# Kernel optimization log

Measured on AMD Instinct MI355X. Metric: run time of the kernel, lower is better.

Reference implementation:

```python
import jax, jax.numpy as jnp
import numpy as np

N = 100000   # nodes
E = 1600000  # edges
R = 8        # relations
B = 8        # bases (min(R, hidden))
IN = 128; HID = 128; OUT = 128
BN_EPS = 1e-5


def setup_inputs() -> dict:
    key = jax.random.key(0)
    ks = jax.random.split(key, 20)
    s = 0.1  # xavier-ish small gain as in reset_parameters
    f32 = jnp.float32
    inp = {
        'x': jax.random.normal(ks[0], (N, IN), f32),
        'edge_index': jax.random.randint(ks[1], (2, E), 0, N, dtype=jnp.int32),
        'edge_type': jax.random.randint(ks[2], (E,), 0, R, dtype=jnp.int32),
        # RGCNConv layer 1 (basis decomposition)
        'basis1': jax.random.normal(ks[3], (B, IN, HID), f32) * s,
        'comp1': jax.random.normal(ks[4], (R, B), f32) * s,
        'root1': jax.random.normal(ks[5], (IN, HID), f32) * s,
        'bias1': jnp.zeros((HID,), f32),
        # layer 2
        'basis2': jax.random.normal(ks[6], (B, HID, HID), f32) * s,
        'comp2': jax.random.normal(ks[7], (R, B), f32) * s,
        'root2': jax.random.normal(ks[8], (HID, HID), f32) * s,
        'bias2': jnp.zeros((HID,), f32),
        # layer 3
        'basis3': jax.random.normal(ks[9], (B, HID, OUT), f32) * s,
        'comp3': jax.random.normal(ks[10], (R, B), f32) * s,
        'root3': jax.random.normal(ks[11], (HID, OUT), f32) * s,
        'bias3': jnp.zeros((OUT,), f32),
        # BatchNorm affine params (batch-stat normalization)
        'bn1_gamma': jnp.ones((HID,), f32),
        'bn1_beta': jnp.zeros((HID,), f32),
        'bn2_gamma': jnp.ones((HID,), f32),
        'bn2_beta': jnp.zeros((HID,), f32),
    }
    return inp


def rgcn_conv(x, basis, comp, root, bias, src, dst, etype):
    # relation weights from basis decomposition: W[r] = sum_b comp[r,b] * basis[b]
    W = jnp.einsum('rb,bio->rio', comp, basis)  # [R, in, out]
    # mean aggregation per (dst, relation); transform after mean (linearity)
    seg = dst.astype(jnp.int32) * R + etype.astype(jnp.int32)  # [E]
    msg_sum = jax.ops.segment_sum(x[src], seg, num_segments=N * R)  # [N*R, in]
    cnt = jax.ops.segment_sum(jnp.ones((src.shape[0],), x.dtype), seg, num_segments=N * R)
    mean = msg_sum / jnp.maximum(cnt, 1.0)[:, None]
    mean = mean.reshape(N, R, -1)  # [N, R, in]
    out = jnp.einsum('nri,rio->no', mean, W) + x @ root + bias
    return out


def batchnorm(h, gamma, beta):
    m = h.mean(axis=0)
    v = h.var(axis=0)
    return (h - m) * jax.lax.rsqrt(v + BN_EPS) * gamma + beta


def reference(x, edge_index, edge_type,
              basis1, comp1, root1, bias1,
              basis2, comp2, root2, bias2,
              basis3, comp3, root3, bias3,
              bn1_gamma, bn1_beta, bn2_gamma, bn2_beta):
    src, dst = edge_index[0], edge_index[1]
    h = rgcn_conv(x, basis1, comp1, root1, bias1, src, dst, edge_type)
    h = batchnorm(h, bn1_gamma, bn1_beta)
    h = jnp.where(h > 0, h, 0.1 * h)  # LeakyReLU(0.1); dropout inactive (eval)
    h = rgcn_conv(h, basis2, comp2, root2, bias2, src, dst, edge_type)
    h = batchnorm(h, bn2_gamma, bn2_beta)
    h = jnp.where(h > 0, h, 0.1 * h)
    h = rgcn_conv(h, basis3, comp3, root3, bias3, src, dst, edge_type)
    # F.normalize(p=2, dim=1)
    norm = jnp.maximum(jnp.sqrt(jnp.sum(h * h, axis=1, keepdims=True)), 1e-12)
    return h / norm
```

## Files before the change

kernel.cpp:

```cpp
#include <hip/hip_runtime.h>

#define NN 100000
#define EE 1600000
#define RRR 8
#define NSEG (NN*RRR)
#define F 128
#define KDIM 1152
#define NKT 36
#define BNEPS 1e-5f

typedef __attribute__((ext_vector_type(8))) short bf16x8;
typedef __attribute__((ext_vector_type(8))) unsigned short u16x8;
typedef __attribute__((ext_vector_type(4))) float f32x4;

static __device__ __forceinline__ unsigned short bf16r(float f) {
  unsigned u = __float_as_uint(f);
  u += 0x7fffu + ((u >> 16) & 1u);
  return (unsigned short)(u >> 16);
}
static __device__ __forceinline__ float b2f(unsigned short s) {
  return __uint_as_float((unsigned)s << 16);
}

__global__ __launch_bounds__(256) void k_precnt(const float* __restrict__ x,
    unsigned short* __restrict__ xb, const int* __restrict__ dst,
    const int* __restrict__ et, unsigned* __restrict__ cnt) {
  int idx = blockIdx.x*256 + threadIdx.x;
  if (idx < NN*32) {
    float4 v = ((const float4*)x)[idx];
    ushort4 o;
    o.x = bf16r(v.x); o.y = bf16r(v.y); o.z = bf16r(v.z); o.w = bf16r(v.w);
    ((ushort4*)xb)[idx] = o;
  }
  if (idx < EE)
    atomicAdd(&cnt[dst[idx]*RRR + et[idx]], 1u);
}

__global__ void k_scan1(const unsigned* __restrict__ cnt, unsigned* __restrict__ off,
                        unsigned* __restrict__ bsum) {
  __shared__ unsigned s[256];
  int t = threadIdx.x;
  int base = blockIdx.x*2048 + t*8;
  unsigned loc[8];
  unsigned tot = 0;
#pragma unroll
  for (int j = 0; j < 8; j++) {
    unsigned v = (base+j < NSEG) ? cnt[base+j] : 0u;
    loc[j] = tot;
    tot += v;
  }
  s[t] = tot;
  __syncthreads();
  for (int d = 1; d < 256; d <<= 1) {
    unsigned v = (t >= d) ? s[t-d] : 0u;
    __syncthreads();
    s[t] += v;
    __syncthreads();
  }
  unsigned tbase = s[t] - tot;
#pragma unroll
  for (int j = 0; j < 8; j++)
    if (base+j < NSEG) off[base+j] = tbase + loc[j];
  if (t == 255) bsum[blockIdx.x] = s[255];
}

__global__ void k_scan2(unsigned* bsum, int nb) {
  __shared__ unsigned s[512];
  int t = threadIdx.x;
  unsigned v = (t < nb) ? bsum[t] : 0u;
  s[t] = v;
  __syncthreads();
  for (int d = 1; d < 512; d <<= 1) {
    unsigned u = (t >= d) ? s[t-d] : 0u;
    __syncthreads();
    s[t] += u;
    __syncthreads();
  }
  if (t < nb) bsum[t] = (t == 0) ? 0u : s[t-1];
}

__global__ void k_scan3(unsigned* off, const unsigned* __restrict__ bsum) {
  int i = blockIdx.x*256 + threadIdx.x;
  if (i < NSEG) off[i] += bsum[i >> 11];
}

__global__ void k_fill(const int* __restrict__ src, const int* __restrict__ dst,
                       const int* __restrict__ et, unsigned* __restrict__ off,
                       int* __restrict__ csr) {
  int e = blockIdx.x*256 + threadIdx.x;
  if (e < EE) {
    int seg = dst[e]*RRR + et[e];
    unsigned pos = atomicAdd(&off[seg], 1u);
    csr[pos] = src[e];
  }
}

__global__ void k_makeW3(const float* __restrict__ b1, const float* __restrict__ c1,
                         const float* __restrict__ r1, const float* __restrict__ b2,
                         const float* __restrict__ c2, const float* __restrict__ r2,
                         const float* __restrict__ b3, const float* __restrict__ c3,
                         const float* __restrict__ r3, unsigned short* __restrict__ WB3,
                         float* __restrict__ stats) {
  int kt = blockIdx.x, ct = blockIdx.y, l = blockIdx.z;
  int lane = threadIdx.x;
  if (kt == 0 && ct == 0 && l == 0) {
#pragma unroll
    for (int j = 0; j < 8; j++) stats[lane*8 + j] = 0.f;
  }
  const float* basis = (l == 0) ? b1 : (l == 1) ? b2 : b3;
  const float* comp  = (l == 0) ? c1 : (l == 1) ? c2 : c3;
  const float* root  = (l == 0) ? r1 : (l == 1) ? r2 : r3;
  int o = ct*16 + (lane & 15);
  int kbase = kt*32 + (lane >> 4)*8;
  unsigned short v[8];
#pragma unroll
  for (int j = 0; j < 8; j++) {
    int k = kbase + j;
    float val;
    if (k < 1024) {
      int r = k >> 7, i = k & 127;
      val = 0.f;
#pragma unroll
      for (int bb = 0; bb < 8; bb++)
        val += comp[r*8+bb] * basis[(bb*F + i)*F + o];
    } else {
      val = root[(k - 1024)*F + o];
    }
    v[j] = bf16r(val);
  }
  unsigned short* dstp = WB3 + (size_t)l*KDIM*F + ((size_t)(kt*8 + ct)*64 + lane)*8;
#pragma unroll
  for (int j = 0; j < 8; j++) dstp[j] = v[j];
}

__global__ __launch_bounds__(256) void k_agg(const unsigned short* __restrict__ hb,
    const unsigned* __restrict__ off, const unsigned* __restrict__ cnt,
    const int* __restrict__ csr, unsigned short* __restrict__ Mean,
    const float* __restrict__ stats, const float* __restrict__ gamma,
    const float* __restrict__ beta, int nodeBase, int hasBN) {
  int t = threadIdx.x;
  int sl = t & 15, c8 = sl*8;
  int g = t >> 4;
  int nl = blockIdx.x*4 + (g & 3);
  int node = nodeBase + nl;
  int rp = g >> 2;
  float sc[8], sh[8];
  float lk = hasBN ? 0.1f : 1.0f;
  if (hasBN) {
    const float invN = 1.f/(float)NN;
#pragma unroll
    for (int u = 0; u < 8; u++) {
      float m = stats[c8+u]*invN;
      float var = stats[128+c8+u]*invN - m*m;
      float rs = rsqrtf(var + BNEPS);
      float gg = gamma[c8+u]*rs;
      sc[u] = gg;
      sh[u] = beta[c8+u] - m*gg;
    }
  } else {
#pragma unroll
    for (int u = 0; u < 8; u++) { sc[u] = 1.f; sh[u] = 0.f; }
  }
  int s0 = node*RRR + 2*rp;
  unsigned cA = cnt[s0], cB = cnt[s0+1];
  unsigned bA = off[s0] - cA, bB = off[s0+1] - cB;
  const unsigned short* hc = hb + c8;
  float aA[8], aB[8];
#pragma unroll
  for (int u = 0; u < 8; u++) { aA[u] = 0.f; aB[u] = 0.f; }
  unsigned jA = 0, jB = 0;
  while (jA < cA || jB < cB) {
    unsigned nA = cA - jA; if (nA > 2) nA = 2;
    unsigned nB = cB - jB; if (nB > 2) nB = 2;
    int i0 = 0, i1 = 0, i2 = 0, i3 = 0;
    if (nA > 0) i0 = csr[bA + jA];
    if (nA > 1) i1 = csr[bA + jA + 1];
    if (nB > 0) i2 = csr[bB + jB];
    if (nB > 1) i3 = csr[bB + jB + 1];
    if (nA > 0) {
      u16x8 v = *(const u16x8*)&hc[(size_t)i0*F];
#pragma unroll
      for (int u = 0; u < 8; u++) { float z = b2f(v[u])*sc[u]+sh[u]; aA[u] += fmaxf(z, lk*z); }
    }
    if (nA > 1) {
      u16x8 v = *(const u16x8*)&hc[(size_t)i1*F];
#pragma unroll
      for (int u = 0; u < 8; u++) { float z = b2f(v[u])*sc[u]+sh[u]; aA[u] += fmaxf(z, lk*z); }
    }
    if (nB > 0) {
      u16x8 v = *(const u16x8*)&hc[(size_t)i2*F];
#pragma unroll
      for (int u = 0; u < 8; u++) { float z = b2f(v[u])*sc[u]+sh[u]; aB[u] += fmaxf(z, lk*z); }
    }
    if (nB > 1) {
      u16x8 v = *(const u16x8*)&hc[(size_t)i3*F];
#pragma unroll
      for (int u = 0; u < 8; u++) { float z = b2f(v[u])*sc[u]+sh[u]; aB[u] += fmaxf(z, lk*z); }
    }
    jA += nA; jB += nB;
  }
  float ivA = cA ? 1.f/(float)cA : 0.f;
  float ivB = cB ? 1.f/(float)cB : 0.f;
  u16x8 oA, oB;
#pragma unroll
  for (int u = 0; u < 8; u++) { oA[u] = bf16r(aA[u]*ivA); oB[u] = bf16r(aB[u]*ivB); }
  int ktl = sl >> 2, kgl = sl & 3;
  int rt = nl >> 4;
  int lraw = (nl & 15) + 16*kgl;
  size_t ciA = ((size_t)(rt*NKT + (2*rp  )*4 + ktl)*64 + lraw)*8;
  size_t ciB = ((size_t)(rt*NKT + (2*rp+1)*4 + ktl)*64 + lraw)*8;
  *(u16x8*)&Mean[ciA] = oA;
  *(u16x8*)&Mean[ciB] = oB;
  if (rp == 0) {
    u16x8 v = *(const u16x8*)&hc[(size_t)node*F];
    u16x8 os;
#pragma unroll
    for (int u = 0; u < 8; u++) {
      float z = b2f(v[u])*sc[u] + sh[u];
      os[u] = bf16r(fmaxf(z, lk*z));
    }
    size_t cs = ((size_t)(rt*NKT + 32 + ktl)*64 + lraw)*8;
    *(u16x8*)&Mean[cs] = os;
  }
}

__global__ __launch_bounds__(256) void k_gemm(const unsigned short* __restrict__ Mean,
    const unsigned short* __restrict__ WB, const float* __restrict__ bias,
    unsigned short* __restrict__ houtb, float* __restrict__ foutp,
    float* __restrict__ stats, int outBase, int count, int mode) {
  __shared__ float s_sum[128];
  __shared__ float s_sq[128];
  int t = threadIdx.x;
  int wave = t >> 6;
  int lane = t & 63;
  int rt = blockIdx.x*4 + wave;
  int rbase = rt*16;
  int rlo = lane & 15;
  int kg = lane >> 4;
  const unsigned short* ap = Mean + ((size_t)rt*NKT*64 + lane)*8;
  const unsigned short* bp = WB + (size_t)lane*8;

  if (mode == 0 && t < 128) { s_sum[t] = 0.f; s_sq[t] = 0.f; }

  f32x4 acc[8];
#pragma unroll
  for (int j = 0; j < 8; j++) acc[j] = (f32x4){0.f,0.f,0.f,0.f};

  for (int kt = 0; kt < NKT; kt++) {
    bf16x8 a = *(const bf16x8*)(ap + (size_t)kt*512);
#pragma unroll
    for (int ct = 0; ct < 8; ct++) {
      bf16x8 b = *(const bf16x8*)(bp + (size_t)(kt*8 + ct)*512);
      acc[ct] = __builtin_amdgcn_mfma_f32_16x16x32_bf16(a, b, acc[ct], 0, 0, 0);
    }
  }

  float bv[8];
#pragma unroll
  for (int ct = 0; ct < 8; ct++) bv[ct] = bias[ct*16 + rlo];

  if (mode == 0) {
    __syncthreads();
    float psum[8], psq[8];
#pragma unroll
    for (int ct = 0; ct < 8; ct++) { psum[ct] = 0.f; psq[ct] = 0.f; }
#pragma unroll
    for (int i = 0; i < 4; i++) {
      int row = rbase + kg*4 + i;
      if (row < count) {
        unsigned short* orow = houtb + (size_t)(outBase + row)*F;
#pragma unroll
        for (int ct = 0; ct < 8; ct++) {
          float y = acc[ct][i] + bv[ct];
          orow[ct*16 + rlo] = bf16r(y);
          psum[ct] += y;
          psq[ct]  += y*y;
        }
      }
    }
#pragma unroll
    for (int ct = 0; ct < 8; ct++) {
      atomicAdd(&s_sum[ct*16 + rlo], psum[ct]);
      atomicAdd(&s_sq [ct*16 + rlo], psq[ct]);
    }
    __syncthreads();
    if (t < 128) {
      atomicAdd(&stats[t],       s_sum[t]);
      atomicAdd(&stats[128 + t], s_sq[t]);
    }
  } else {
#pragma unroll
    for (int i = 0; i < 4; i++) {
      int row = rbase + kg*4 + i;
      float y[8], ss = 0.f;
#pragma unroll
      for (int ct = 0; ct < 8; ct++) {
        y[ct] = acc[ct][i] + bv[ct];
        ss += y[ct]*y[ct];
      }
#pragma unroll
      for (int m = 1; m < 16; m <<= 1)
        ss += __shfl_xor(ss, m, 64);
      float inv = 1.f / fmaxf(sqrtf(ss), 1e-12f);
      if (row < count) {
        float* orow = foutp + (size_t)(outBase + row)*F;
#pragma unroll
        for (int ct = 0; ct < 8; ct++)
          orow[ct*16 + rlo] = y[ct]*inv;
      }
    }
  }
}

extern "C" void kernel_launch(void* const* d_in, const int* in_sizes, int n_in,
                              void* d_out, int out_size, void* d_ws, size_t ws_size,
                              hipStream_t stream) {
  const float* x      = (const float*)d_in[0];
  const int*   ei     = (const int*)d_in[1];
  const int*   etp    = (const int*)d_in[2];
  const float* basis[3] = {(const float*)d_in[3], (const float*)d_in[7],  (const float*)d_in[11]};
  const float* comp[3]  = {(const float*)d_in[4], (const float*)d_in[8],  (const float*)d_in[12]};
  const float* root[3]  = {(const float*)d_in[5], (const float*)d_in[9],  (const float*)d_in[13]};
  const float* bias[3]  = {(const float*)d_in[6], (const float*)d_in[10], (const float*)d_in[14]};
  const float* gamma[2] = {(const float*)d_in[15], (const float*)d_in[17]};
  const float* beta[2]  = {(const float*)d_in[16], (const float*)d_in[18]};
  const int* srcv = ei;
  const int* dstv = ei + EE;
  float* out = (float*)d_out;

  char* w = (char*)d_ws;
  size_t p = 0;
  auto take = [&](size_t bytes) -> void* {
    void* q = w + p;
    p = (p + bytes + 255) & ~(size_t)255;
    return q;
  };
  unsigned* cnt   = (unsigned*)take((size_t)NSEG*4);
  unsigned* off   = (unsigned*)take((size_t)NSEG*4);
  int*      csr   = (int*)     take((size_t)EE*4);
  unsigned* bsum  = (unsigned*)take(1024*4);
  unsigned short* WB3 = (unsigned short*)take((size_t)3*KDIM*F*2);
  float*    stats = (float*)   take(512*4);
  unsigned short* hbuf0 = (unsigned short*)take((size_t)NN*F*2);
  unsigned short* hbuf1 = (unsigned short*)take((size_t)NN*F*2);
  unsigned short* xb    = (unsigned short*)take((size_t)NN*F*2);
  size_t avail = (ws_size > p) ? (ws_size - p) : 0;
  long long rows = (long long)(avail / ((size_t)KDIM*2)) - 64;
  int CH = (rows > NN) ? NN : (int)(rows & ~63LL);
  if (CH < 64) CH = 64;
  unsigned short* Mean = (unsigned short*)(w + p);

  hipMemsetAsync(cnt, 0, (size_t)NSEG*4, stream);
  k_precnt<<<12500, 256, 0, stream>>>(x, xb, dstv, etp, cnt);
  int nb1 = (NSEG + 2047)/2048;
  k_scan1<<<nb1, 256, 0, stream>>>(cnt, off, bsum);
  k_scan2<<<1, 512, 0, stream>>>(bsum, nb1);
  k_scan3<<<(NSEG+255)/256, 256, 0, stream>>>(off, bsum);
  k_fill<<<(EE+255)/256, 256, 0, stream>>>(srcv, dstv, etp, off, csr);
  dim3 gw(NKT, 8, 3);
  k_makeW3<<<gw, 64, 0, stream>>>(basis[0], comp[0], root[0],
                                  basis[1], comp[1], root[1],
                                  basis[2], comp[2], root[2], WB3, stats);

  for (int l = 0; l < 3; l++) {
    const unsigned short* hin = (l == 0) ? xb : ((l == 1) ? hbuf0 : hbuf1);
    unsigned short* hout = (l == 0) ? hbuf0 : hbuf1;
    const unsigned short* WB = WB3 + (size_t)l*KDIM*F;
    int mode = (l == 2) ? 1 : 0;
    float* st_out = stats + (size_t)(l < 2 ? l : 0)*256;
    const float* st_in = (l > 0) ? (stats + (size_t)(l-1)*256) : stats;
    const float* gm = (l > 0) ? gamma[l-1] : gamma[0];
    const float* bt = (l > 0) ? beta[l-1]  : beta[0];
    for (int b0n = 0; b0n < NN; b0n += CH) {
      int cc = NN - b0n; if (cc > CH) cc = CH;
      k_agg<<<cc/4, 256, 0, stream>>>(hin, off, cnt, csr, Mean, st_in, gm, bt, b0n, l > 0);
      k_gemm<<<(cc+63)/64, 256, 0, stream>>>(Mean, WB, bias[l], hout, out, st_out, b0n, cc, mode);
    }
  }
}
```

Baseline: 1.096 ms.

## Transform node features per relation before aggregating, replacing the aggregate-then-GEMM flow

Reorders each RGCN layer to transform first, then aggregate. A small GEMM computes per-relation transformed tables Y_r = h·W_r plus the root transform for every node, and a gather kernel averages the Y_r rows over each node's incoming edges, adding bias. The GEMM's K dimension drops from 1152 to 128. BatchNorm+LeakyReLU moves into the GEMM's input load, and the BN scale/shift is precomputed by a tiny kernel. The aim is to remove the large Mean buffer round-trip and the wide GEMM, at the cost of random gathers over a table nine times larger, which may cache worse. If workspace is short, the work is split into chunks using an fp32 accumulator in the output buffer.

```diff
diff --git a/kernel.cpp b/kernel.cpp
--- a/kernel.cpp
+++ b/kernel.cpp
@@ -5,8 +5,6 @@
 #define RRR 8
 #define NSEG (NN*RRR)
 #define F 128
-#define KDIM 1152
-#define NKT 36
 #define BNEPS 1e-5f
 
 typedef __attribute__((ext_vector_type(8))) short bf16x8;
@@ -22,18 +20,10 @@
   return __uint_as_float((unsigned)s << 16);
 }
 
-__global__ __launch_bounds__(256) void k_precnt(const float* __restrict__ x,
-    unsigned short* __restrict__ xb, const int* __restrict__ dst,
-    const int* __restrict__ et, unsigned* __restrict__ cnt) {
-  int idx = blockIdx.x*256 + threadIdx.x;
-  if (idx < NN*32) {
-    float4 v = ((const float4*)x)[idx];
-    ushort4 o;
-    o.x = bf16r(v.x); o.y = bf16r(v.y); o.z = bf16r(v.z); o.w = bf16r(v.w);
-    ((ushort4*)xb)[idx] = o;
-  }
-  if (idx < EE)
-    atomicAdd(&cnt[dst[idx]*RRR + et[idx]], 1u);
+__global__ void k_cnt(const int* __restrict__ dst, const int* __restrict__ et,
+                      unsigned* __restrict__ cnt) {
+  int e = blockIdx.x*256 + threadIdx.x;
+  if (e < EE) atomicAdd(&cnt[dst[e]*RRR + et[e]], 1u);
 }
 
 __global__ void k_scan1(const unsigned* __restrict__ cnt, unsigned* __restrict__ off,
@@ -111,177 +101,243 @@
   const float* comp  = (l == 0) ? c1 : (l == 1) ? c2 : c3;
   const float* root  = (l == 0) ? r1 : (l == 1) ? r2 : r3;
   int o = ct*16 + (lane & 15);
+  int rr = o >> 7, oc = o & 127;
   int kbase = kt*32 + (lane >> 4)*8;
   unsigned short v[8];
 #pragma unroll
   for (int j = 0; j < 8; j++) {
     int k = kbase + j;
     float val;
-    if (k < 1024) {
-      int r = k >> 7, i = k & 127;
+    if (rr < 8) {
       val = 0.f;
 #pragma unroll
       for (int bb = 0; bb < 8; bb++)
-        val += comp[r*8+bb] * basis[(bb*F + i)*F + o];
+        val += comp[rr*8+bb] * basis[(bb*F + k)*F + oc];
     } else {
-      val = root[(k - 1024)*F + o];
+      val = root[k*F + oc];
     }
     v[j] = bf16r(val);
   }
-  unsigned short* dstp = WB3 + (size_t)l*KDIM*F + ((size_t)(kt*8 + ct)*64 + lane)*8;
+  unsigned short* dstp = WB3 + (size_t)l*(F*1152) + ((size_t)(kt*72 + ct)*64 + lane)*8;
 #pragma unroll
   for (int j = 0; j < 8; j++) dstp[j] = v[j];
 }
 
-__global__ __launch_bounds__(256) void k_agg(const unsigned short* __restrict__ hb,
+__global__ void k_scsh(const float* __restrict__ stats, const float* __restrict__ gamma,
+                       const float* __restrict__ beta, float* __restrict__ scsh) {
+  int c = threadIdx.x;
+  const float invN = 1.f/(float)NN;
+  float m = stats[c]*invN;
+  float var = stats[128+c]*invN - m*m;
+  float rs = rsqrtf(var + BNEPS);
+  float g = gamma[c]*rs;
+  scsh[c] = g;
+  scsh[128+c] = beta[c] - m*g;
+}
+
+__global__ __launch_bounds__(256) void k_gemmY(const float* __restrict__ xin,
+    const unsigned short* __restrict__ cin, const float* __restrict__ scsh,
+    const unsigned short* __restrict__ WB, unsigned short* __restrict__ Yb,
+    int useF32, int ct0, int ct1, int tb0) {
+  int t = threadIdx.x;
+  int wave = t >> 6, lane = t & 63;
+  int rlo = lane & 15, kg = lane >> 4;
+  int rbase = (blockIdx.x*4 + wave)*32;
+  int r0 = rbase + rlo;       if (r0 > NN-1) r0 = NN-1;
+  int r1 = rbase + 16 + rlo;  if (r1 > NN-1) r1 = NN-1;
+
+  bf16x8 a0[4], a1[4];
+#pragma unroll
+  for (int kt = 0; kt < 4; kt++) {
+    int co = kt*32 + kg*8;
+    u16x8 o0, o1;
+    if (useF32) {
+      const float* p0 = xin + (size_t)r0*F + co;
+      const float* p1 = xin + (size_t)r1*F + co;
+      float4 v0a = *(const float4*)p0, v0b = *(const float4*)(p0+4);
+      float4 v1a = *(const float4*)p1, v1b = *(const float4*)(p1+4);
+      o0[0]=bf16r(v0a.x); o0[1]=bf16r(v0a.y); o0[2]=bf16r(v0a.z); o0[3]=bf16r(v0a.w);
+      o0[4]=bf16r(v0b.x); o0[5]=bf16r(v0b.y); o0[6]=bf16r(v0b.z); o0[7]=bf16r(v0b.w);
+      o1[0]=bf16r(v1a.x); o1[1]=bf16r(v1a.y); o1[2]=bf16r(v1a.z); o1[3]=bf16r(v1a.w);
+      o1[4]=bf16r(v1b.x); o1[5]=bf16r(v1b.y); o1[6]=bf16r(v1b.z); o1[7]=bf16r(v1b.w);
+    } else {
+      u16x8 v0 = *(const u16x8*)&cin[(size_t)r0*F + co];
+      u16x8 v1 = *(const u16x8*)&cin[(size_t)r1*F + co];
+      float4 sca = *(const float4*)&scsh[co], scb = *(const float4*)&scsh[co+4];
+      float4 sha = *(const float4*)&scsh[128+co], shb = *(const float4*)&scsh[128+co+4];
+      float sc[8] = {sca.x,sca.y,sca.z,sca.w,scb.x,scb.y,scb.z,scb.w};
+      float sh[8] = {sha.x,sha.y,sha.z,sha.w,shb.x,shb.y,shb.z,shb.w};
+#pragma unroll
+      for (int j = 0; j < 8; j++) {
+        float z0 = b2f(v0[j])*sc[j] + sh[j];
+        float z1 = b2f(v1[j])*sc[j] + sh[j];
+        o0[j] = bf16r(fmaxf(z0, 0.1f*z0));
+        o1[j] = bf16r(fmaxf(z1, 0.1f*z1));
+      }
+    }
+    a0[kt] = (bf16x8)o0;
+    a1[kt] = (bf16x8)o1;
+  }
+
+  const unsigned short* bp = WB + (size_t)lane*8;
+  for (int ct = ct0; ct < ct1; ct++) {
+    f32x4 acc0 = (f32x4){0.f,0.f,0.f,0.f};
+    f32x4 acc1 = (f32x4){0.f,0.f,0.f,0.f};
+#pragma unroll
+    for (int kt = 0; kt < 4; kt++) {
+      bf16x8 b = *(const bf16x8*)(bp + (size_t)(kt*72 + ct)*512);
+      acc0 = __builtin_amdgcn_mfma_f32_16x16x32_bf16(a0[kt], b, acc0, 0, 0, 0);
+      acc1 = __builtin_amdgcn_mfma_f32_16x16x32_bf16(a1[kt], b, acc1, 0, 0, 0);
+    }
+    int rr = (ct >> 3) - tb0;
+    int oc = (ct & 7)*16 + rlo;
+    unsigned short* yb = Yb + (size_t)rr*NN*F + oc;
+#pragma unroll
+    for (int i = 0; i < 4; i++) {
+      int n0 = rbase + kg*4 + i;
+      int n1 = rbase + 16 + kg*4 + i;
+      if (n0 < NN) yb[(size_t)n0*F] = bf16r(acc0[i]);
+      if (n1 < NN) yb[(size_t)n1*F] = bf16r(acc1[i]);
+    }
+  }
+}
+
+__global__ __launch_bounds__(256) void k_aggC(const unsigned short* __restrict__ Yb,
     const unsigned* __restrict__ off, const unsigned* __restrict__ cnt,
-    const int* __restrict__ csr, unsigned short* __restrict__ Mean,
-    const float* __restrict__ stats, const float* __restrict__ gamma,
-    const float* __restrict__ beta, int nodeBase, int hasBN) {
+    const int* __restrict__ csr, const float* __restrict__ bias,
+    unsigned short* __restrict__ cbuf, float* __restrict__ accb,
+    float* __restrict__ fout, float* __restrict__ stats,
+    int tb0, int ntab, int mode, int first, int last) {
+  __shared__ float s_sum[128], s_sq[128];
   int t = threadIdx.x;
   int sl = t & 15, c8 = sl*8;
   int g = t >> 4;
-  int nl = blockIdx.x*4 + (g & 3);
-  int node = nodeBase + nl;
-  int rp = g >> 2;
-  float sc[8], sh[8];
-  float lk = hasBN ? 0.1f : 1.0f;
-  if (hasBN) {
-    const float invN = 1.f/(float)NN;
+  int lane = t & 63;
+  int node = blockIdx.x*16 + g;
+  if (mode == 0 && last && t < 128) { s_sum[t] = 0.f; s_sq[t] = 0.f; }
+
+  float a[8];
+  if (first) {
+    float4 ba = *(const float4*)&bias[c8];
+    float4 bb = *(const float4*)&bias[c8+4];
+    a[0]=ba.x; a[1]=ba.y; a[2]=ba.z; a[3]=ba.w;
+    a[4]=bb.x; a[5]=bb.y; a[6]=bb.z; a[7]=bb.w;
+  } else {
+    const float* ap = accb + (size_t)node*F + c8;
+    float4 va = *(const float4*)ap;
+    float4 vb = *(const float4*)(ap+4);
+    a[0]=va.x; a[1]=va.y; a[2]=va.z; a[3]=va.w;
+    a[4]=vb.x; a[5]=vb.y; a[6]=vb.z; a[7]=vb.w;
+  }
+
+  int rend = tb0 + ntab;
+  int relEnd = (rend < 8) ? rend : 8;
+  int r = tb0;
+  while (r < relEnd) {
+    if (r + 1 < relEnd) {
+      int s0 = node*RRR + r;
+      unsigned cA = cnt[s0], cB = cnt[s0+1];
+      unsigned bA = off[s0] - cA, bB = off[s0+1] - cB;
+      const unsigned short* tA = Yb + (size_t)(r - tb0)*NN*F + c8;
+      const unsigned short* tB = tA + (size_t)NN*F;
+      float sA[8], sB[8];
+#pragma unroll
+      for (int u = 0; u < 8; u++) { sA[u] = 0.f; sB[u] = 0.f; }
+      unsigned jA = 0, jB = 0;
+      while (jA < cA || jB < cB) {
+        unsigned nA = cA - jA; if (nA > 2) nA = 2;
+        unsigned nB = cB - jB; if (nB > 2) nB = 2;
+        int i0 = 0, i1 = 0, i2 = 0, i3 = 0;
+        if (nA > 0) i0 = csr[bA + jA];
+        if (nA > 1) i1 = csr[bA + jA + 1];
+        if (nB > 0) i2 = csr[bB + jB];
+        if (nB > 1) i3 = csr[bB + jB + 1];
+        if (nA > 0) {
+          u16x8 v = *(const u16x8*)&tA[(size_t)i0*F];
+#pragma unroll
+          for (int u = 0; u < 8; u++) sA[u] += b2f(v[u]);
+        }
+        if (nA > 1) {
+          u16x8 v = *(const u16x8*)&tA[(size_t)i1*F];
+#pragma unroll
+          for (int u = 0; u < 8; u++) sA[u] += b2f(v[u]);
+        }
+        if (nB > 0) {
+          u16x8 v = *(const u16x8*)&tB[(size_t)i2*F];
+#pragma unroll
+          for (int u = 0; u < 8; u++) sB[u] += b2f(v[u]);
+        }
+        if (nB > 1) {
+          u16x8 v = *(const u16x8*)&tB[(size_t)i3*F];
+#pragma unroll
+          for (int u = 0; u < 8; u++) sB[u] += b2f(v[u]);
+        }
+        jA += nA; jB += nB;
+      }
+      float ivA = cA ? 1.f/(float)cA : 0.f;
+      float ivB = cB ? 1.f/(float)cB : 0.f;
+#pragma unroll
+      for (int u = 0; u < 8; u++) a[u] += sA[u]*ivA + sB[u]*ivB;
+      r += 2;
+    } else {
+      int s0 = node*RRR + r;
+      unsigned cA = cnt[s0];
+      unsigned bA = off[s0] - cA;
+      const unsigned short* tA = Yb + (size_t)(r - tb0)*NN*F + c8;
+      float sA[8];
+#pragma unroll
+      for (int u = 0; u < 8; u++) sA[u] = 0.f;
+      unsigned j = 0;
+      for (; j + 2 <= cA; j += 2) {
+        int i0 = csr[bA + j];
+        int i1 = csr[bA + j + 1];
+        u16x8 v0 = *(const u16x8*)&tA[(size_t)i0*F];
+        u16x8 v1 = *(const u16x8*)&tA[(size_t)i1*F];
+#pragma unroll
+        for (int u = 0; u < 8; u++) sA[u] += b2f(v0[u]) + b2f(v1[u]);
+      }
+      if (j < cA) {
+        int i0 = csr[bA + j];
+        u16x8 v0 = *(const u16x8*)&tA[(size_t)i0*F];
+#pragma unroll
+        for (int u = 0; u < 8; u++) sA[u] += b2f(v0[u]);
+      }
+      float ivA = cA ? 1.f/(float)cA : 0.f;
+#pragma unroll
+      for (int u = 0; u < 8; u++) a[u] += sA[u]*ivA;
+      r += 1;
+    }
+  }
+  if (rend > 8) {
+    u16x8 v = *(const u16x8*)&Yb[((size_t)(8 - tb0)*NN + node)*F + c8];
+#pragma unroll
+    for (int u = 0; u < 8; u++) a[u] += b2f(v[u]);
+  }
+
+  if (!last) {
+    float* ap = accb + (size_t)node*F + c8;
+    *(float4*)ap     = make_float4(a[0], a[1], a[2], a[3]);
+    *(float4*)(ap+4) = make_float4(a[4], a[5], a[6], a[7]);
+  } else if (mode == 0) {
+    u16x8 o;
+#pragma unroll
+    for (int u = 0; u < 8; u++) o[u] = bf16r(a[u]);
+    *(u16x8*)&cbuf[(size_t)node*F + c8] = o;
+    float ps[8], pq[8];
+#pragma unroll
+    for (int u = 0; u < 8; u++) { ps[u] = a[u]; pq[u] = a[u]*a[u]; }
 #pragma unroll
     for (int u = 0; u < 8; u++) {
-      float m = stats[c8+u]*invN;
-      float var = stats[128+c8+u]*invN - m*m;
-      float rs = rsqrtf(var + BNEPS);
-      float gg = gamma[c8+u]*rs;
-      sc[u] = gg;
-      sh[u] = beta[c8+u] - m*gg;
-    }
-  } else {
-#pragma unroll
-    for (int u = 0; u < 8; u++) { sc[u] = 1.f; sh[u] = 0.f; }
-  }
-  int s0 = node*RRR + 2*rp;
-  unsigned cA = cnt[s0], cB = cnt[s0+1];
-  unsigned bA = off[s0] - cA, bB = off[s0+1] - cB;
-  const unsigned short* hc = hb + c8;
-  float aA[8], aB[8];
-#pragma unroll
-  for (int u = 0; u < 8; u++) { aA[u] = 0.f; aB[u] = 0.f; }
-  unsigned jA = 0, jB = 0;
-  while (jA < cA || jB < cB) {
-    unsigned nA = cA - jA; if (nA > 2) nA = 2;
-    unsigned nB = cB - jB; if (nB > 2) nB = 2;
-    int i0 = 0, i1 = 0, i2 = 0, i3 = 0;
-    if (nA > 0) i0 = csr[bA + jA];
-    if (nA > 1) i1 = csr[bA + jA + 1];
-    if (nB > 0) i2 = csr[bB + jB];
-    if (nB > 1) i3 = csr[bB + jB + 1];
-    if (nA > 0) {
-      u16x8 v = *(const u16x8*)&hc[(size_t)i0*F];
-#pragma unroll
-      for (int u = 0; u < 8; u++) { float z = b2f(v[u])*sc[u]+sh[u]; aA[u] += fmaxf(z, lk*z); }
-    }
-    if (nA > 1) {
-      u16x8 v = *(const u16x8*)&hc[(size_t)i1*F];
-#pragma unroll
-      for (int u = 0; u < 8; u++) { float z = b2f(v[u])*sc[u]+sh[u]; aA[u] += fmaxf(z, lk*z); }
-    }
-    if (nB > 0) {
-      u16x8 v = *(const u16x8*)&hc[(size_t)i2*F];
-#pragma unroll
-      for (int u = 0; u < 8; u++) { float z = b2f(v[u])*sc[u]+sh[u]; aB[u] += fmaxf(z, lk*z); }
-    }
-    if (nB > 1) {
-      u16x8 v = *(const u16x8*)&hc[(size_t)i3*F];
-#pragma unroll
-      for (int u = 0; u < 8; u++) { float z = b2f(v[u])*sc[u]+sh[u]; aB[u] += fmaxf(z, lk*z); }
-    }
-    jA += nA; jB += nB;
-  }
-  float ivA = cA ? 1.f/(float)cA : 0.f;
-  float ivB = cB ? 1.f/(float)cB : 0.f;
-  u16x8 oA, oB;
-#pragma unroll
-  for (int u = 0; u < 8; u++) { oA[u] = bf16r(aA[u]*ivA); oB[u] = bf16r(aB[u]*ivB); }
-  int ktl = sl >> 2, kgl = sl & 3;
-  int rt = nl >> 4;
-  int lraw = (nl & 15) + 16*kgl;
-  size_t ciA = ((size_t)(rt*NKT + (2*rp  )*4 + ktl)*64 + lraw)*8;
-  size_t ciB = ((size_t)(rt*NKT + (2*rp+1)*4 + ktl)*64 + lraw)*8;
-  *(u16x8*)&Mean[ciA] = oA;
-  *(u16x8*)&Mean[ciB] = oB;
-  if (rp == 0) {
-    u16x8 v = *(const u16x8*)&hc[(size_t)node*F];
-    u16x8 os;
-#pragma unroll
-    for (int u = 0; u < 8; u++) {
-      float z = b2f(v[u])*sc[u] + sh[u];
-      os[u] = bf16r(fmaxf(z, lk*z));
-    }
-    size_t cs = ((size_t)(rt*NKT + 32 + ktl)*64 + lraw)*8;
-    *(u16x8*)&Mean[cs] = os;
-  }
-}
-
-__global__ __launch_bounds__(256) void k_gemm(const unsigned short* __restrict__ Mean,
-    const unsigned short* __restrict__ WB, const float* __restrict__ bias,
-    unsigned short* __restrict__ houtb, float* __restrict__ foutp,
-    float* __restrict__ stats, int outBase, int count, int mode) {
-  __shared__ float s_sum[128];
-  __shared__ float s_sq[128];
-  int t = threadIdx.x;
-  int wave = t >> 6;
-  int lane = t & 63;
-  int rt = blockIdx.x*4 + wave;
-  int rbase = rt*16;
-  int rlo = lane & 15;
-  int kg = lane >> 4;
-  const unsigned short* ap = Mean + ((size_t)rt*NKT*64 + lane)*8;
-  const unsigned short* bp = WB + (size_t)lane*8;
-
-  if (mode == 0 && t < 128) { s_sum[t] = 0.f; s_sq[t] = 0.f; }
-
-  f32x4 acc[8];
-#pragma unroll
-  for (int j = 0; j < 8; j++) acc[j] = (f32x4){0.f,0.f,0.f,0.f};
-
-  for (int kt = 0; kt < NKT; kt++) {
-    bf16x8 a = *(const bf16x8*)(ap + (size_t)kt*512);
-#pragma unroll
-    for (int ct = 0; ct < 8; ct++) {
-      bf16x8 b = *(const bf16x8*)(bp + (size_t)(kt*8 + ct)*512);
-      acc[ct] = __builtin_amdgcn_mfma_f32_16x16x32_bf16(a, b, acc[ct], 0, 0, 0);
-    }
-  }
-
-  float bv[8];
-#pragma unroll
-  for (int ct = 0; ct < 8; ct++) bv[ct] = bias[ct*16 + rlo];
-
-  if (mode == 0) {
-    __syncthreads();
-    float psum[8], psq[8];
-#pragma unroll
-    for (int ct = 0; ct < 8; ct++) { psum[ct] = 0.f; psq[ct] = 0.f; }
-#pragma unroll
-    for (int i = 0; i < 4; i++) {
-      int row = rbase + kg*4 + i;
-      if (row < count) {
-        unsigned short* orow = houtb + (size_t)(outBase + row)*F;
-#pragma unroll
-        for (int ct = 0; ct < 8; ct++) {
-          float y = acc[ct][i] + bv[ct];
-          orow[ct*16 + rlo] = bf16r(y);
-          psum[ct] += y;
-          psq[ct]  += y*y;
-        }
+      ps[u] += __shfl_xor(ps[u], 16, 64); ps[u] += __shfl_xor(ps[u], 32, 64);
+      pq[u] += __shfl_xor(pq[u], 16, 64); pq[u] += __shfl_xor(pq[u], 32, 64);
+    }
+    __syncthreads();
+    if (lane < 16) {
+#pragma unroll
+      for (int u = 0; u < 8; u++) {
+        atomicAdd(&s_sum[c8+u], ps[u]);
+        atomicAdd(&s_sq [c8+u], pq[u]);
       }
-    }
-#pragma unroll
-    for (int ct = 0; ct < 8; ct++) {
-      atomicAdd(&s_sum[ct*16 + rlo], psum[ct]);
-      atomicAdd(&s_sq [ct*16 + rlo], psq[ct]);
     }
     __syncthreads();
     if (t < 128) {
@@ -289,26 +345,15 @@
       atomicAdd(&stats[128 + t], s_sq[t]);
     }
   } else {
-#pragma unroll
-    for (int i = 0; i < 4; i++) {
-      int row = rbase + kg*4 + i;
-      float y[8], ss = 0.f;
-#pragma unroll
-      for (int ct = 0; ct < 8; ct++) {
-        y[ct] = acc[ct][i] + bv[ct];
-        ss += y[ct]*y[ct];
-      }
-#pragma unroll
-      for (int m = 1; m < 16; m <<= 1)
-        ss += __shfl_xor(ss, m, 64);
-      float inv = 1.f / fmaxf(sqrtf(ss), 1e-12f);
-      if (row < count) {
-        float* orow = foutp + (size_t)(outBase + row)*F;
-#pragma unroll
-        for (int ct = 0; ct < 8; ct++)
-          orow[ct*16 + rlo] = y[ct]*inv;
-      }
-    }
+    float ss = 0.f;
+#pragma unroll
+    for (int u = 0; u < 8; u++) ss += a[u]*a[u];
+    ss += __shfl_xor(ss, 1, 64); ss += __shfl_xor(ss, 2, 64);
+    ss += __shfl_xor(ss, 4, 64); ss += __shfl_xor(ss, 8, 64);
+    float inv = 1.f / fmaxf(sqrtf(ss), 1e-12f);
+    float* orow = fout + (size_t)node*F + c8;
+    *(float4*)orow     = make_float4(a[0]*inv, a[1]*inv, a[2]*inv, a[3]*inv);
+    *(float4*)(orow+4) = make_float4(a[4]*inv, a[5]*inv, a[6]*inv, a[7]*inv);
   }
 }
 
@@ -339,42 +384,46 @@
   unsigned* off   = (unsigned*)take((size_t)NSEG*4);
   int*      csr   = (int*)     take((size_t)EE*4);
   unsigned* bsum  = (unsigned*)take(1024*4);
-  unsigned short* WB3 = (unsigned short*)take((size_t)3*KDIM*F*2);
+  unsigned short* WB3 = (unsigned short*)take((size_t)3*F*1152*2);
   float*    stats = (float*)   take(512*4);
-  unsigned short* hbuf0 = (unsigned short*)take((size_t)NN*F*2);
-  unsigned short* hbuf1 = (unsigned short*)take((size_t)NN*F*2);
-  unsigned short* xb    = (unsigned short*)take((size_t)NN*F*2);
+  float*    scshb = (float*)   take(512*4);
+  unsigned short* cbuf = (unsigned short*)take((size_t)NN*F*2);
   size_t avail = (ws_size > p) ? (ws_size - p) : 0;
-  long long rows = (long long)(avail / ((size_t)KDIM*2)) - 64;
-  int CH = (rows > NN) ? NN : (int)(rows & ~63LL);
-  if (CH < 64) CH = 64;
-  unsigned short* Mean = (unsigned short*)(w + p);
+  size_t tabBytes = (size_t)NN*F*2;
+  int ntab = (int)(avail / tabBytes);
+  if (ntab > 9) ntab = 9;
+  if (ntab < 1) ntab = 1;
+  unsigned short* Yb = (unsigned short*)(w + p);
 
   hipMemsetAsync(cnt, 0, (size_t)NSEG*4, stream);
-  k_precnt<<<12500, 256, 0, stream>>>(x, xb, dstv, etp, cnt);
+  k_cnt<<<(EE+255)/256, 256, 0, stream>>>(dstv, etp, cnt);
   int nb1 = (NSEG + 2047)/2048;
   k_scan1<<<nb1, 256, 0, stream>>>(cnt, off, bsum);
   k_scan2<<<1, 512, 0, stream>>>(bsum, nb1);
   k_scan3<<<(NSEG+255)/256, 256, 0, stream>>>(off, bsum);
   k_fill<<<(EE+255)/256, 256, 0, stream>>>(srcv, dstv, etp, off, csr);
-  dim3 gw(NKT, 8, 3);
+  dim3 gw(4, 72, 3);
   k_makeW3<<<gw, 64, 0, stream>>>(basis[0], comp[0], root[0],
                                   basis[1], comp[1], root[1],
                                   basis[2], comp[2], root[2], WB3, stats);
 
+  int gemmBlocks = (NN + 127)/128;
+  int aggBlocks  = NN/16;
   for (int l = 0; l < 3; l++) {
-    const unsigned short* hin = (l == 0) ? xb : ((l == 1) ? hbuf0 : hbuf1);
-    unsigned short* hout = (l == 0) ? hbuf0 : hbuf1;
-    const unsigned short* WB = WB3 + (size_t)l*KDIM*F;
+    const unsigned short* WB = WB3 + (size_t)l*F*1152;
+    const float* sc = (l > 0) ? (scshb + (size_t)(l-1)*256) : scshb;
+    float* st = (l < 2) ? (stats + (size_t)l*256) : stats;
     int mode = (l == 2) ? 1 : 0;
-    float* st_out = stats + (size_t)(l < 2 ? l : 0)*256;
-    const float* st_in = (l > 0) ? (stats + (size_t)(l-1)*256) : stats;
-    const float* gm = (l > 0) ? gamma[l-1] : gamma[0];
-    const float* bt = (l > 0) ? beta[l-1]  : beta[0];
-    for (int b0n = 0; b0n < NN; b0n += CH) {
-      int cc = NN - b0n; if (cc > CH) cc = CH;
-      k_agg<<<cc/4, 256, 0, stream>>>(hin, off, cnt, csr, Mean, st_in, gm, bt, b0n, l > 0);
-      k_gemm<<<(cc+63)/64, 256, 0, stream>>>(Mean, WB, bias[l], hout, out, st_out, b0n, cc, mode);
-    }
-  }
-}
+    for (int tb0 = 0; tb0 < 9; tb0 += ntab) {
+      int nt = 9 - tb0; if (nt > ntab) nt = ntab;
+      k_gemmY<<<gemmBlocks, 256, 0, stream>>>(x, cbuf, sc, WB, Yb, l == 0,
+                                              tb0*8, (tb0 + nt)*8, tb0);
+      int first = (tb0 == 0);
+      int last  = (tb0 + nt == 9);
+      k_aggC<<<aggBlocks, 256, 0, stream>>>(Yb, off, cnt, csr, bias[l], cbuf,
+                                            out, out, st, tb0, nt, mode, first, last);
+    }
+    if (l < 2)
+      k_scsh<<<1, 128, 0, stream>>>(st, gamma[l], beta[l], scshb + (size_t)l*256);
+  }
+}
```

New measurement: 1.385 ms. 26.3% more time.

## Fuse per-layer aggregation and GEMM into one kernel via LDS-staged tile

Applied to the files above, without the earlier changes.

Merges the gather-mean aggregation kernel and the MFMA GEMM into a single kernel per layer. Each block aggregates 16 nodes into a swizzled LDS A-tile, then four waves each compute two output column tiles from it. This removes the global Mean round-trip (about 1152 bf16 values per node) and the chunked launch loop. In exchange, each block handles only 16 rows, so every block re-reads the full weight matrix from cache, and the single-wave-per-node gather may lower memory-level parallelism.

```diff
diff --git a/kernel.cpp b/kernel.cpp
--- a/kernel.cpp
+++ b/kernel.cpp
@@ -133,25 +133,31 @@
   for (int j = 0; j < 8; j++) dstp[j] = v[j];
 }
 
-__global__ __launch_bounds__(256) void k_agg(const unsigned short* __restrict__ hb,
+__global__ __launch_bounds__(256) void k_fused(const unsigned short* __restrict__ hb,
     const unsigned* __restrict__ off, const unsigned* __restrict__ cnt,
-    const int* __restrict__ csr, unsigned short* __restrict__ Mean,
-    const float* __restrict__ stats, const float* __restrict__ gamma,
-    const float* __restrict__ beta, int nodeBase, int hasBN) {
+    const int* __restrict__ csr, const unsigned short* __restrict__ WB,
+    const float* __restrict__ bias, const float* __restrict__ statsIn,
+    const float* __restrict__ gamma, const float* __restrict__ beta, int hasBN,
+    unsigned short* __restrict__ houtb, float* __restrict__ fout,
+    float* __restrict__ statsOut, int mode) {
+  __shared__ unsigned short lA[NKT*64*8];
+  __shared__ float s_sum[128], s_sq[128];
+  __shared__ float rowss[16];
   int t = threadIdx.x;
-  int sl = t & 15, c8 = sl*8;
-  int g = t >> 4;
-  int nl = blockIdx.x*4 + (g & 3);
-  int node = nodeBase + nl;
-  int rp = g >> 2;
+  if (mode == 0) { if (t < 128) { s_sum[t] = 0.f; s_sq[t] = 0.f; } }
+  else if (t < 16) rowss[t] = 0.f;
+
+  int g = t >> 4, sl = t & 15, c8 = sl*8;
+  int node = blockIdx.x*16 + g;
+
   float sc[8], sh[8];
   float lk = hasBN ? 0.1f : 1.0f;
   if (hasBN) {
     const float invN = 1.f/(float)NN;
 #pragma unroll
     for (int u = 0; u < 8; u++) {
-      float m = stats[c8+u]*invN;
-      float var = stats[128+c8+u]*invN - m*m;
+      float m = statsIn[c8+u]*invN;
+      float var = statsIn[128+c8+u]*invN - m*m;
       float rs = rsqrtf(var + BNEPS);
       float gg = gamma[c8+u]*rs;
       sc[u] = gg;
@@ -161,57 +167,60 @@
 #pragma unroll
     for (int u = 0; u < 8; u++) { sc[u] = 1.f; sh[u] = 0.f; }
   }
-  int s0 = node*RRR + 2*rp;
-  unsigned cA = cnt[s0], cB = cnt[s0+1];
-  unsigned bA = off[s0] - cA, bB = off[s0+1] - cB;
+
+  int ktl = sl >> 2, kgl = sl & 3;
+  int swz = ((ktl & 1) << 2) | kgl;
+  int rowp = (g ^ swz) + 16*kgl;
   const unsigned short* hc = hb + c8;
-  float aA[8], aB[8];
-#pragma unroll
-  for (int u = 0; u < 8; u++) { aA[u] = 0.f; aB[u] = 0.f; }
-  unsigned jA = 0, jB = 0;
-  while (jA < cA || jB < cB) {
-    unsigned nA = cA - jA; if (nA > 2) nA = 2;
-    unsigned nB = cB - jB; if (nB > 2) nB = 2;
-    int i0 = 0, i1 = 0, i2 = 0, i3 = 0;
-    if (nA > 0) i0 = csr[bA + jA];
-    if (nA > 1) i1 = csr[bA + jA + 1];
-    if (nB > 0) i2 = csr[bB + jB];
-    if (nB > 1) i3 = csr[bB + jB + 1];
-    if (nA > 0) {
-      u16x8 v = *(const u16x8*)&hc[(size_t)i0*F];
-#pragma unroll
-      for (int u = 0; u < 8; u++) { float z = b2f(v[u])*sc[u]+sh[u]; aA[u] += fmaxf(z, lk*z); }
-    }
-    if (nA > 1) {
-      u16x8 v = *(const u16x8*)&hc[(size_t)i1*F];
-#pragma unroll
-      for (int u = 0; u < 8; u++) { float z = b2f(v[u])*sc[u]+sh[u]; aA[u] += fmaxf(z, lk*z); }
-    }
-    if (nB > 0) {
-      u16x8 v = *(const u16x8*)&hc[(size_t)i2*F];
-#pragma unroll
-      for (int u = 0; u < 8; u++) { float z = b2f(v[u])*sc[u]+sh[u]; aB[u] += fmaxf(z, lk*z); }
-    }
-    if (nB > 1) {
-      u16x8 v = *(const u16x8*)&hc[(size_t)i3*F];
-#pragma unroll
-      for (int u = 0; u < 8; u++) { float z = b2f(v[u])*sc[u]+sh[u]; aB[u] += fmaxf(z, lk*z); }
-    }
-    jA += nA; jB += nB;
-  }
-  float ivA = cA ? 1.f/(float)cA : 0.f;
-  float ivB = cB ? 1.f/(float)cB : 0.f;
-  u16x8 oA, oB;
-#pragma unroll
-  for (int u = 0; u < 8; u++) { oA[u] = bf16r(aA[u]*ivA); oB[u] = bf16r(aB[u]*ivB); }
-  int ktl = sl >> 2, kgl = sl & 3;
-  int rt = nl >> 4;
-  int lraw = (nl & 15) + 16*kgl;
-  size_t ciA = ((size_t)(rt*NKT + (2*rp  )*4 + ktl)*64 + lraw)*8;
-  size_t ciB = ((size_t)(rt*NKT + (2*rp+1)*4 + ktl)*64 + lraw)*8;
-  *(u16x8*)&Mean[ciA] = oA;
-  *(u16x8*)&Mean[ciB] = oB;
-  if (rp == 0) {
+
+#pragma unroll
+  for (int rp = 0; rp < 4; rp++) {
+    int s0 = node*RRR + 2*rp;
+    unsigned cA = cnt[s0], cB = cnt[s0+1];
+    unsigned bA = off[s0] - cA, bB = off[s0+1] - cB;
+    float aA[8], aB[8];
+#pragma unroll
+    for (int u = 0; u < 8; u++) { aA[u] = 0.f; aB[u] = 0.f; }
+    unsigned jA = 0, jB = 0;
+    while (jA < cA || jB < cB) {
+      unsigned nA = cA - jA; if (nA > 2) nA = 2;
+      unsigned nB = cB - jB; if (nB > 2) nB = 2;
+      int i0 = 0, i1 = 0, i2 = 0, i3 = 0;
+      if (nA > 0) i0 = csr[bA + jA];
+      if (nA > 1) i1 = csr[bA + jA + 1];
+      if (nB > 0) i2 = csr[bB + jB];
+      if (nB > 1) i3 = csr[bB + jB + 1];
+      if (nA > 0) {
+        u16x8 v = *(const u16x8*)&hc[(size_t)i0*F];
+#pragma unroll
+        for (int u = 0; u < 8; u++) { float z = b2f(v[u])*sc[u]+sh[u]; aA[u] += fmaxf(z, lk*z); }
+      }
+      if (nA > 1) {
+        u16x8 v = *(const u16x8*)&hc[(size_t)i1*F];
+#pragma unroll
+        for (int u = 0; u < 8; u++) { float z = b2f(v[u])*sc[u]+sh[u]; aA[u] += fmaxf(z, lk*z); }
+      }
+      if (nB > 0) {
+        u16x8 v = *(const u16x8*)&hc[(size_t)i2*F];
+#pragma unroll
+        for (int u = 0; u < 8; u++) { float z = b2f(v[u])*sc[u]+sh[u]; aB[u] += fmaxf(z, lk*z); }
+      }
+      if (nB > 1) {
+        u16x8 v = *(const u16x8*)&hc[(size_t)i3*F];
+#pragma unroll
+        for (int u = 0; u < 8; u++) { float z = b2f(v[u])*sc[u]+sh[u]; aB[u] += fmaxf(z, lk*z); }
+      }
+      jA += nA; jB += nB;
+    }
+    float ivA = cA ? 1.f/(float)cA : 0.f;
+    float ivB = cB ? 1.f/(float)cB : 0.f;
+    u16x8 oA, oB;
+#pragma unroll
+    for (int u = 0; u < 8; u++) { oA[u] = bf16r(aA[u]*ivA); oB[u] = bf16r(aB[u]*ivB); }
+    *(u16x8*)&lA[((2*rp*4 + ktl)*64 + rowp)*8] = oA;
+    *(u16x8*)&lA[(((2*rp+1)*4 + ktl)*64 + rowp)*8] = oB;
+  }
+  {
     u16x8 v = *(const u16x8*)&hc[(size_t)node*F];
     u16x8 os;
 #pragma unroll
@@ -219,95 +228,86 @@
       float z = b2f(v[u])*sc[u] + sh[u];
       os[u] = bf16r(fmaxf(z, lk*z));
     }
-    size_t cs = ((size_t)(rt*NKT + 32 + ktl)*64 + lraw)*8;
-    *(u16x8*)&Mean[cs] = os;
-  }
-}
-
-__global__ __launch_bounds__(256) void k_gemm(const unsigned short* __restrict__ Mean,
-    const unsigned short* __restrict__ WB, const float* __restrict__ bias,
-    unsigned short* __restrict__ houtb, float* __restrict__ foutp,
-    float* __restrict__ stats, int outBase, int count, int mode) {
-  __shared__ float s_sum[128];
-  __shared__ float s_sq[128];
-  int t = threadIdx.x;
-  int wave = t >> 6;
-  int lane = t & 63;
-  int rt = blockIdx.x*4 + wave;
-  int rbase = rt*16;
-  int rlo = lane & 15;
-  int kg = lane >> 4;
-  const unsigned short* ap = Mean + ((size_t)rt*NKT*64 + lane)*8;
-  const unsigned short* bp = WB + (size_t)lane*8;
-
-  if (mode == 0 && t < 128) { s_sum[t] = 0.f; s_sq[t] = 0.f; }
-
-  f32x4 acc[8];
-#pragma unroll
-  for (int j = 0; j < 8; j++) acc[j] = (f32x4){0.f,0.f,0.f,0.f};
-
+    *(u16x8*)&lA[((32 + ktl)*64 + rowp)*8] = os;
+  }
+  __syncthreads();
+
+  int wave = t >> 6, lane = t & 63;
+  int rlo = lane & 15, kg = lane >> 4;
+  int ct0 = wave*2;
+  f32x4 acc0 = (f32x4){0.f,0.f,0.f,0.f};
+  f32x4 acc1 = (f32x4){0.f,0.f,0.f,0.f};
+#pragma unroll 4
   for (int kt = 0; kt < NKT; kt++) {
-    bf16x8 a = *(const bf16x8*)(ap + (size_t)kt*512);
-#pragma unroll
-    for (int ct = 0; ct < 8; ct++) {
-      bf16x8 b = *(const bf16x8*)(bp + (size_t)(kt*8 + ct)*512);
-      acc[ct] = __builtin_amdgcn_mfma_f32_16x16x32_bf16(a, b, acc[ct], 0, 0, 0);
-    }
-  }
-
-  float bv[8];
-#pragma unroll
-  for (int ct = 0; ct < 8; ct++) bv[ct] = bias[ct*16 + rlo];
+    int sw = ((kt & 1) << 2) | kg;
+    bf16x8 a = *(const bf16x8*)&lA[((size_t)kt*64 + ((rlo ^ sw) + 16*kg))*8];
+    const unsigned short* bp = WB + ((size_t)(kt*8 + ct0)*64 + lane)*8;
+    bf16x8 b0 = *(const bf16x8*)bp;
+    bf16x8 b1 = *(const bf16x8*)(bp + 512);
+    acc0 = __builtin_amdgcn_mfma_f32_16x16x32_bf16(a, b0, acc0, 0, 0, 0);
+    acc1 = __builtin_amdgcn_mfma_f32_16x16x32_bf16(a, b1, acc1, 0, 0, 0);
+  }
+
+  float bv0 = bias[ct0*16 + rlo];
+  float bv1 = bias[(ct0+1)*16 + rlo];
+  int rbase = blockIdx.x*16;
 
   if (mode == 0) {
-    __syncthreads();
-    float psum[8], psq[8];
-#pragma unroll
-    for (int ct = 0; ct < 8; ct++) { psum[ct] = 0.f; psq[ct] = 0.f; }
+    float psum0 = 0.f, psq0 = 0.f, psum1 = 0.f, psq1 = 0.f;
 #pragma unroll
     for (int i = 0; i < 4; i++) {
       int row = rbase + kg*4 + i;
-      if (row < count) {
-        unsigned short* orow = houtb + (size_t)(outBase + row)*F;
-#pragma unroll
-        for (int ct = 0; ct < 8; ct++) {
-          float y = acc[ct][i] + bv[ct];
-          orow[ct*16 + rlo] = bf16r(y);
-          psum[ct] += y;
-          psq[ct]  += y*y;
-        }
-      }
-    }
-#pragma unroll
-    for (int ct = 0; ct < 8; ct++) {
-      atomicAdd(&s_sum[ct*16 + rlo], psum[ct]);
-      atomicAdd(&s_sq [ct*16 + rlo], psq[ct]);
+      float y0 = acc0[i] + bv0;
+      float y1 = acc1[i] + bv1;
+      unsigned short* orow = houtb + (size_t)row*F;
+      orow[ct0*16 + rlo]     = bf16r(y0);
+      orow[(ct0+1)*16 + rlo] = bf16r(y1);
+      psum0 += y0; psq0 += y0*y0;
+      psum1 += y1; psq1 += y1*y1;
+    }
+    psum0 += __shfl_xor(psum0, 16, 64); psum0 += __shfl_xor(psum0, 32, 64);
+    psq0  += __shfl_xor(psq0 , 16, 64); psq0  += __shfl_xor(psq0 , 32, 64);
+    psum1 += __shfl_xor(psum1, 16, 64); psum1 += __shfl_xor(psum1, 32, 64);
+    psq1  += __shfl_xor(psq1 , 16, 64); psq1  += __shfl_xor(psq1 , 32, 64);
+    if (lane < 16) {
+      atomicAdd(&s_sum[ct0*16 + rlo], psum0);
+      atomicAdd(&s_sq [ct0*16 + rlo], psq0);
+      atomicAdd(&s_sum[(ct0+1)*16 + rlo], psum1);
+      atomicAdd(&s_sq [(ct0+1)*16 + rlo], psq1);
     }
     __syncthreads();
     if (t < 128) {
-      atomicAdd(&stats[t],       s_sum[t]);
-      atomicAdd(&stats[128 + t], s_sq[t]);
+      atomicAdd(&statsOut[t],       s_sum[t]);
+      atomicAdd(&statsOut[128 + t], s_sq[t]);
     }
   } else {
+    float y0v[4], y1v[4], ssp[4];
+#pragma unroll
+    for (int i = 0; i < 4; i++) {
+      y0v[i] = acc0[i] + bv0;
+      y1v[i] = acc1[i] + bv1;
+      ssp[i] = y0v[i]*y0v[i] + y1v[i]*y1v[i];
+    }
+#pragma unroll
+    for (int i = 0; i < 4; i++) {
+      ssp[i] += __shfl_xor(ssp[i], 1, 64);
+      ssp[i] += __shfl_xor(ssp[i], 2, 64);
+      ssp[i] += __shfl_xor(ssp[i], 4, 64);
+      ssp[i] += __shfl_xor(ssp[i], 8, 64);
+    }
+    if (rlo == 0) {
+#pragma unroll
+      for (int i = 0; i < 4; i++)
+        atomicAdd(&rowss[kg*4 + i], ssp[i]);
+    }
+    __syncthreads();
 #pragma unroll
     for (int i = 0; i < 4; i++) {
       int row = rbase + kg*4 + i;
-      float y[8], ss = 0.f;
-#pragma unroll
-      for (int ct = 0; ct < 8; ct++) {
-        y[ct] = acc[ct][i] + bv[ct];
-        ss += y[ct]*y[ct];
-      }
-#pragma unroll
-      for (int m = 1; m < 16; m <<= 1)
-        ss += __shfl_xor(ss, m, 64);
-      float inv = 1.f / fmaxf(sqrtf(ss), 1e-12f);
-      if (row < count) {
-        float* orow = foutp + (size_t)(outBase + row)*F;
-#pragma unroll
-        for (int ct = 0; ct < 8; ct++)
-          orow[ct*16 + rlo] = y[ct]*inv;
-      }
+      float inv = 1.f / fmaxf(sqrtf(rowss[kg*4 + i]), 1e-12f);
+      float* orow = fout + (size_t)row*F;
+      orow[ct0*16 + rlo]     = y0v[i]*inv;
+      orow[(ct0+1)*16 + rlo] = y1v[i]*inv;
     }
   }
 }
@@ -341,14 +341,10 @@
   unsigned* bsum  = (unsigned*)take(1024*4);
   unsigned short* WB3 = (unsigned short*)take((size_t)3*KDIM*F*2);
   float*    stats = (float*)   take(512*4);
-  unsigned short* hbuf0 = (unsigned short*)take((size_t)NN*F*2);
-  unsigned short* hbuf1 = (unsigned short*)take((size_t)NN*F*2);
   unsigned short* xb    = (unsigned short*)take((size_t)NN*F*2);
-  size_t avail = (ws_size > p) ? (ws_size - p) : 0;
-  long long rows = (long long)(avail / ((size_t)KDIM*2)) - 64;
-  int CH = (rows > NN) ? NN : (int)(rows & ~63LL);
-  if (CH < 64) CH = 64;
-  unsigned short* Mean = (unsigned short*)(w + p);
+  unsigned short* cbuf0 = (unsigned short*)take((size_t)NN*F*2);
+  unsigned short* cbuf1 = (unsigned short*)take((size_t)NN*F*2);
+  (void)ws_size;
 
   hipMemsetAsync(cnt, 0, (size_t)NSEG*4, stream);
   k_precnt<<<12500, 256, 0, stream>>>(x, xb, dstv, etp, cnt);
@@ -362,19 +358,14 @@
                                   basis[1], comp[1], root[1],
                                   basis[2], comp[2], root[2], WB3, stats);
 
-  for (int l = 0; l < 3; l++) {
-    const unsigned short* hin = (l == 0) ? xb : ((l == 1) ? hbuf0 : hbuf1);
-    unsigned short* hout = (l == 0) ? hbuf0 : hbuf1;
-    const unsigned short* WB = WB3 + (size_t)l*KDIM*F;
-    int mode = (l == 2) ? 1 : 0;
-    float* st_out = stats + (size_t)(l < 2 ? l : 0)*256;
-    const float* st_in = (l > 0) ? (stats + (size_t)(l-1)*256) : stats;
-    const float* gm = (l > 0) ? gamma[l-1] : gamma[0];
-    const float* bt = (l > 0) ? beta[l-1]  : beta[0];
-    for (int b0n = 0; b0n < NN; b0n += CH) {
-      int cc = NN - b0n; if (cc > CH) cc = CH;
-      k_agg<<<cc/4, 256, 0, stream>>>(hin, off, cnt, csr, Mean, st_in, gm, bt, b0n, l > 0);
-      k_gemm<<<(cc+63)/64, 256, 0, stream>>>(Mean, WB, bias[l], hout, out, st_out, b0n, cc, mode);
-    }
-  }
-}
+  int NB = NN/16;
+  k_fused<<<NB, 256, 0, stream>>>(xb, off, cnt, csr, WB3, bias[0],
+                                  stats, gamma[0], beta[0], 0,
+                                  cbuf0, out, stats, 0);
+  k_fused<<<NB, 256, 0, stream>>>(cbuf0, off, cnt, csr, WB3 + (size_t)KDIM*F, bias[1],
+                                  stats, gamma[0], beta[0], 1,
+                                  cbuf1, out, stats + 256, 0);
+  k_fused<<<NB, 256, 0, stream>>>(cbuf1, off, cnt, csr, WB3 + (size_t)2*KDIM*F, bias[2],
+                                  stats + 256, gamma[1], beta[1], 1,
+                                  cbuf0, out, stats, 1);
+}
```

Measured after the change: 965.8 us. -11.9%, faster.
